# Optimization experiments

Hardware: AMD Instinct MI355X
Metric: run time of the kernel (lower is better)

## Reference

```python
import jax, jax.numpy as jnp
import numpy as np

OBJECT_NUM = 512
ATTRIBUTES_NUM = 8
E_DIMS = 256


def setup_inputs() -> dict:
    key = jax.random.key(0)
    k1, k2 = jax.random.split(key)
    x = jax.random.normal(k1, (64, 2048), dtype=jnp.float32)
    E_absolute_position = jax.random.normal(k2, (OBJECT_NUM, E_DIMS), dtype=jnp.float32)
    return {"x": x, "E_absolute_position": E_absolute_position}


def reference(x, E_absolute_position):
    batch_size, seq_len = x.shape[0], x.shape[1]
    # token index -> object index via floor division (same as int(token/attributes_num))
    idx = jnp.arange(seq_len) // ATTRIBUTES_NUM          # [S]
    rows = E_absolute_position[idx]                       # [S, E]
    out = jnp.broadcast_to(rows[None, :, :], (batch_size, seq_len, E_DIMS))
    return out
```

## Files before the change

### kernel.cpp

```cpp
#include <hip/hip_runtime.h>
#include <hip/hip_bf16.h>


constexpr unsigned BATCH       = 64;
constexpr unsigned SEQ         = 2048;
constexpr unsigned EDIM        = 256;
constexpr unsigned VEC_PER_ROW = EDIM / 4;
constexpr unsigned TOTAL_VEC   = BATCH * SEQ * VEC_PER_ROW;

__global__ __launch_bounds__(256)
void ape_broadcast_kernel(const float4* __restrict__ E, float4* __restrict__ out) {
    unsigned v   = blockIdx.x * blockDim.x + threadIdx.x;
    unsigned e4  = v & (VEC_PER_ROW - 1);
    unsigned row = v >> 6;
    unsigned s   = row & (SEQ - 1);
    unsigned obj = s >> 3;
    out[v] = E[obj * VEC_PER_ROW + e4];
}

extern "C" void kernel_launch(void* const* d_in, const int* in_sizes, int n_in,
                              void* d_out, int out_size, void* d_ws, size_t ws_size,
                              hipStream_t stream) {
    const float4* E = (const float4*)d_in[1];
    float4* out     = (float4*)d_out;

    constexpr unsigned BLOCK = 256;
    constexpr unsigned GRID  = TOTAL_VEC / BLOCK;
    ape_broadcast_kernel<<<GRID, BLOCK, 0, stream>>>(E, out);
}
```

Before: 132.6 us.

## Load each row once and store it to 16 batches with nontemporal writes

Each thread now reads its embedding vector once and writes it to 16 batch planes, using a 2D grid where y covers groups of batches. This removes redundant loads and index math per output element and cuts block count 16x. Stores use nontemporal hints to avoid polluting cache with the 128MB write-only output. The cost is fewer, longer-running blocks, which may reduce memory-level parallelism.

```diff
diff --git a/kernel.cpp b/kernel.cpp
--- a/kernel.cpp
+++ b/kernel.cpp
@@ -1,30 +1,41 @@
 #include <hip/hip_runtime.h>
-#include <hip/hip_bf16.h>
 
 
-constexpr unsigned BATCH       = 64;
-constexpr unsigned SEQ         = 2048;
-constexpr unsigned EDIM        = 256;
-constexpr unsigned VEC_PER_ROW = EDIM / 4;
-constexpr unsigned TOTAL_VEC   = BATCH * SEQ * VEC_PER_ROW;
+typedef float floatx4 __attribute__((ext_vector_type(4)));
 
-__global__ __launch_bounds__(256)
-void ape_broadcast_kernel(const float4* __restrict__ E, float4* __restrict__ out) {
-    unsigned v   = blockIdx.x * blockDim.x + threadIdx.x;
+constexpr unsigned BATCH           = 64;
+constexpr unsigned SEQ             = 2048;
+constexpr unsigned EDIM            = 256;
+constexpr unsigned VEC_PER_ROW     = EDIM / 4;
+constexpr unsigned PLANE_VEC       = SEQ * VEC_PER_ROW;
+constexpr unsigned BLOCK           = 256;
+constexpr unsigned BATCH_PER_BLOCK = 16;
+
+__global__ __launch_bounds__(BLOCK)
+void ape_broadcast_kernel(const floatx4* __restrict__ E, floatx4* __restrict__ out) {
+    unsigned v   = blockIdx.x * BLOCK + threadIdx.x;
     unsigned e4  = v & (VEC_PER_ROW - 1);
-    unsigned row = v >> 6;
-    unsigned s   = row & (SEQ - 1);
+    unsigned s   = v >> 6;
     unsigned obj = s >> 3;
-    out[v] = E[obj * VEC_PER_ROW + e4];
+
+    floatx4 val = E[obj * VEC_PER_ROW + e4];
+
+    unsigned b0 = blockIdx.y * BATCH_PER_BLOCK;
+    floatx4* p  = out + (size_t)b0 * PLANE_VEC + v;
+#pragma unroll
+    for (unsigned i = 0; i < BATCH_PER_BLOCK; ++i) {
+        __builtin_nontemporal_store(val, p);
+        p += PLANE_VEC;
+    }
 }
 
 extern "C" void kernel_launch(void* const* d_in, const int* in_sizes, int n_in,
                               void* d_out, int out_size, void* d_ws, size_t ws_size,
                               hipStream_t stream) {
-    const float4* E = (const float4*)d_in[1];
-    float4* out     = (float4*)d_out;
+    const floatx4* E = (const floatx4*)d_in[1];
+    floatx4* out     = (floatx4*)d_out;
 
-    constexpr unsigned BLOCK = 256;
-    constexpr unsigned GRID  = TOTAL_VEC / BLOCK;
-    ape_broadcast_kernel<<<GRID, BLOCK, 0, stream>>>(E, out);
+    dim3 grid(PLANE_VEC / BLOCK,
+              BATCH / BATCH_PER_BLOCK);
+    ape_broadcast_kernel<<<grid, dim3(BLOCK), 0, stream>>>(E, out);
 }
```

After: 140.5 us. +6.0%, slower.
